# Kernel optimization log

Hardware: AMD Instinct MI355X
Metric: run time of the kernel (lower is better)

## Reference

```python
import jax, jax.numpy as jnp
import numpy as np

TEMPERATURE = 0.5
EPS = 1e-8  # matches F.cosine_similarity eps clamp


def setup_inputs() -> dict:
    key = jax.random.key(0)
    k1, k2 = jax.random.split(key)
    logits = jax.random.normal(k1, (8192, 256), dtype=jnp.float32)
    label = jax.random.randint(k2, (8192,), 0, 10, dtype=jnp.int64)
    return {"logits": logits, "label": label}


def reference(logits, label):
    n = label.shape[0]
    # pairwise cosine similarity via normalize + GEMM (same math as the
    # broadcasted F.cosine_similarity, without the O(n^2 d) intermediate)
    norms = jnp.maximum(jnp.linalg.norm(logits, axis=1, keepdims=True), EPS)
    xn = logits / norms                       # [n, d]
    sim_matrix = xn @ xn.T                    # [n, n]

    eye = jnp.eye(n, dtype=sim_matrix.dtype)
    mask = (label[:, None] == label[None, :]).astype(sim_matrix.dtype)  # same-label (incl. diag)

    e = jnp.exp(sim_matrix / TEMPERATURE) * (1.0 - eye)  # zero diagonal
    sim = mask * e                            # same-label positives
    no_sim_sum = jnp.sum(e - sim, axis=1)     # [n] row sums of different-label terms
    sim_sum = sim + no_sim_sum[:, None]       # denominator per entry
    ratio = sim / sim_sum

    # zeros (different-label entries) get +1 via (1 - mask), diagonal gets +1 via eye -> -log(1) = 0
    loss_mat = -jnp.log((1.0 - mask) + ratio + eye)
    return jnp.sum(loss_mat) / (2 * n)
```

## Files before the change

kernel.cpp:

```cpp
#include <hip/hip_runtime.h>
#include <cstdint>
#include <cstddef>

typedef __bf16 bf16x8 __attribute__((ext_vector_type(8)));
typedef float  f32x4  __attribute__((ext_vector_type(4)));

#define N_ROWS 8192
#define KDIM   256
#define TEMP_INV 2.0f
#define LOG2E  1.4426950408889634f
#define EXPC   (TEMP_INV * LOG2E)

__device__ __forceinline__ ushort f2bf(float x) {
    uint32_t u = __float_as_uint(x);
    u += 0x7fffu + ((u >> 16) & 1u);
    return (ushort)(u >> 16);
}

__global__ void build_perm(const int* __restrict__ label, int* __restrict__ perm,
                           int* __restrict__ labelPerm, int* __restrict__ classStart,
                           int* __restrict__ cumTiles)
{
    __shared__ int lcnt[256][10];
    __shared__ int cstart[11];
    __shared__ int ccount[10];
    const int tid = threadIdx.x;
    const int wave = tid >> 6, lane = tid & 63;
    const int beg = tid * 32, end = beg + 32;

    int loc[10] = {0,0,0,0,0,0,0,0,0,0};
    for (int i = beg; i < end; ++i) {
        int c = label[i]; c = (c < 0) ? 0 : (c > 9 ? 9 : c);
        loc[c]++;
    }
    #pragma unroll
    for (int c = 0; c < 10; ++c) lcnt[tid][c] = loc[c];
    __syncthreads();

    for (int c = wave; c < 10; c += 4) {
        int s0 = lcnt[lane*4+0][c], s1 = lcnt[lane*4+1][c];
        int s2 = lcnt[lane*4+2][c], s3 = lcnt[lane*4+3][c];
        int tot = s0 + s1 + s2 + s3;
        int incl = tot;
        #pragma unroll
        for (int d = 1; d < 64; d <<= 1) {
            int up = __shfl_up(incl, d, 64);
            if (lane >= d) incl += up;
        }
        int excl = incl - tot;
        lcnt[lane*4+0][c] = excl;
        lcnt[lane*4+1][c] = excl + s0;
        lcnt[lane*4+2][c] = excl + s0 + s1;
        lcnt[lane*4+3][c] = excl + s0 + s1 + s2;
        if (lane == 63) ccount[c] = incl;
    }
    __syncthreads();

    if (tid == 0) {
        int run = 0, runT = 0;
        for (int c = 0; c < 10; ++c) {
            cstart[c] = run; classStart[c] = run;
            int tpc = (ccount[c] + 127) >> 7;
            cumTiles[c] = runT;
            run  += ccount[c];
            runT += tpc * tpc;
        }
        cstart[10] = run; classStart[10] = run; cumTiles[10] = runT;
    }
    __syncthreads();

    int ofs[10];
    #pragma unroll
    for (int c = 0; c < 10; ++c) ofs[c] = lcnt[tid][c];
    for (int i = beg; i < end; ++i) {
        int c = label[i]; c = (c < 0) ? 0 : (c > 9 ? 9 : c);
        int pos = cstart[c] + ofs[c]++;
        perm[pos] = i;
        labelPerm[pos] = c;
    }
}

__global__ __launch_bounds__(256) void normalize_rows(const float* __restrict__ logits,
        const int* __restrict__ perm, ushort* __restrict__ xn)
{
    const int p = blockIdx.x * 4 + (threadIdx.x >> 6);
    const int lane = threadIdx.x & 63;
    const int old = perm[p];
    float4 v = reinterpret_cast<const float4*>(logits + (size_t)old * KDIM)[lane];
    float ss = v.x*v.x + v.y*v.y + v.z*v.z + v.w*v.w;
    #pragma unroll
    for (int off = 32; off >= 1; off >>= 1) ss += __shfl_xor(ss, off, 64);
    float inv = 1.0f / fmaxf(sqrtf(ss), 1e-8f);
    ushort4 o;
    o.x = f2bf(v.x * inv); o.y = f2bf(v.y * inv);
    o.z = f2bf(v.z * inv); o.w = f2bf(v.w * inv);
    reinterpret_cast<ushort4*>(xn + (size_t)p * KDIM)[lane] = o;
}

__device__ __forceinline__ void stage_tiles(const ushort* __restrict__ xn,
        int rowBase, int colBase, int kb, ushort* As, ushort* Bs, int wave, int lane)
{
    #pragma unroll
    for (int it = 0; it < 4; ++it) {
        int ci = it * 256 + wave * 64 + lane;
        int row = ci >> 3;
        int c = (ci & 7) ^ (row & 7);
        int rowA = rowBase + row; if (rowA > N_ROWS - 1) rowA = N_ROWS - 1;
        int rowB = colBase + row; if (rowB > N_ROWS - 1) rowB = N_ROWS - 1;
        const ushort* gA = xn + (size_t)rowA * KDIM + kb + c * 8;
        const ushort* gB = xn + (size_t)rowB * KDIM + kb + c * 8;
        ushort* lA = As + (size_t)(it * 256 + wave * 64) * 8;
        ushort* lB = Bs + (size_t)(it * 256 + wave * 64) * 8;
        __builtin_amdgcn_global_load_lds((const __attribute__((address_space(1))) void*)gA,
                                         (__attribute__((address_space(3))) void*)lA, 16, 0, 0);
        __builtin_amdgcn_global_load_lds((const __attribute__((address_space(1))) void*)gB,
                                         (__attribute__((address_space(3))) void*)lB, 16, 0, 0);
    }
}

__device__ __forceinline__ void read_frags(const ushort* As, const ushort* Bs,
        bf16x8 (&a)[2][4], bf16x8 (&b)[2][4], int wave, int lane)
{
    const int wr = wave >> 1, wc = wave & 1;
    const int lrow = lane & 15, kgrp = lane >> 4;
    #pragma unroll
    for (int kk = 0; kk < 2; ++kk) {
        const int c = kk * 4 + kgrp;
        #pragma unroll
        for (int mi = 0; mi < 4; ++mi) {
            const int row = wr*64 + mi*16 + lrow;
            a[kk][mi] = *reinterpret_cast<const bf16x8*>(As + (size_t)row * 64 + ((c ^ (row & 7)) * 8));
        }
        #pragma unroll
        for (int ni = 0; ni < 4; ++ni) {
            const int row = wc*64 + ni*16 + lrow;
            b[kk][ni] = *reinterpret_cast<const bf16x8*>(Bs + (size_t)row * 64 + ((c ^ (row & 7)) * 8));
        }
    }
}

__device__ __forceinline__ void mfma_frags(bf16x8 (&a)[2][4], bf16x8 (&b)[2][4],
                                           f32x4 (&acc)[4][4])
{
    #pragma unroll
    for (int kk = 0; kk < 2; ++kk)
        #pragma unroll
        for (int mi = 0; mi < 4; ++mi)
            #pragma unroll
            for (int ni = 0; ni < 4; ++ni)
                acc[mi][ni] = __builtin_amdgcn_mfma_f32_16x16x32_bf16(a[kk][mi], b[kk][ni], acc[mi][ni], 0, 0, 0);
}

#define PIPE_READS_RELEASE(Ac, Bc)                                   \
    bf16x8 a[2][4], b[2][4];                                         \
    read_frags(Ac, Bc, a, b, wave, lane);                            \
    __builtin_amdgcn_sched_barrier(0);                               \
    asm volatile("s_waitcnt lgkmcnt(0)" ::: "memory");               \
    __builtin_amdgcn_s_barrier();

#define PIPE_MFMA()                                                  \
    __builtin_amdgcn_s_setprio(1);                                   \
    mfma_frags(a, b, acc);                                           \
    __builtin_amdgcn_s_setprio(0);

#define PIPE_TAIL(N)                                                 \
    __builtin_amdgcn_sched_barrier(0);                               \
    asm volatile("s_waitcnt vmcnt(" #N ")" ::: "memory");            \
    __builtin_amdgcn_s_barrier();

__device__ __forceinline__ void kloop_pipe(const ushort* __restrict__ xn,
        int rowBase, int colBase, f32x4 (&acc)[4][4],
        ushort* As0, ushort* Bs0, ushort* As1, ushort* Bs1, int wave, int lane)
{
    stage_tiles(xn, rowBase, colBase, 0,  As0, Bs0, wave, lane);
    stage_tiles(xn, rowBase, colBase, 64, As1, Bs1, wave, lane);
    asm volatile("s_waitcnt vmcnt(8)" ::: "memory");
    __builtin_amdgcn_s_barrier();
    {
        PIPE_READS_RELEASE(As0, Bs0)
        stage_tiles(xn, rowBase, colBase, 128, As0, Bs0, wave, lane);
        PIPE_MFMA()
        PIPE_TAIL(8)
    }
    {
        PIPE_READS_RELEASE(As1, Bs1)
        stage_tiles(xn, rowBase, colBase, 192, As1, Bs1, wave, lane);
        PIPE_MFMA()
        PIPE_TAIL(8)
    }
    {
        PIPE_READS_RELEASE(As0, Bs0)
        PIPE_MFMA()
        PIPE_TAIL(0)
    }
    {
        PIPE_READS_RELEASE(As1, Bs1)
        PIPE_MFMA()
    }
}

__global__ __launch_bounds__(256) void phase1_gemm(const ushort* __restrict__ xn,
        const int* __restrict__ labelPerm, float* __restrict__ pD)
{
    __shared__ __align__(16) char pool[65536];
    ushort* As0 = (ushort*)(pool);
    ushort* Bs0 = (ushort*)(pool + 16384);
    ushort* As1 = (ushort*)(pool + 32768);
    ushort* Bs1 = (ushort*)(pool + 49152);
    float* rowD = (float*)(pool);
    float* colD = (float*)(pool + 16384);
    __shared__ int labLDS[256];

    const int tid = threadIdx.x;
    const int wave = tid >> 6, lane = tid & 63;

    int t = blockIdx.x, bi = 0;
    while (t >= 64 - bi) { t -= 64 - bi; ++bi; }
    const int bj = bi + t;
    const bool isDiag = (bi == bj);
    const int rowBase = bi * 128, colBase = bj * 128;

    labLDS[tid] = labelPerm[(tid < 128) ? (rowBase + tid) : (colBase + tid - 128)];
    __builtin_amdgcn_sched_barrier(0);

    f32x4 acc[4][4] = {};
    kloop_pipe(xn, rowBase, colBase, acc, As0, Bs0, As1, Bs1, wave, lane);

    const int wr = wave >> 1, wc = wave & 1;
    const int lrow = lane & 15, lgrp = lane >> 4;
    float colAcc[4] = {0.f, 0.f, 0.f, 0.f};
    #pragma unroll
    for (int mi = 0; mi < 4; ++mi) {
        #pragma unroll
        for (int reg = 0; reg < 4; ++reg) {
            const int tr = wr * 64 + mi * 16 + lgrp * 4 + reg;
            const int rl = labLDS[tr];
            float rowAcc = 0.f;
            #pragma unroll
            for (int ni = 0; ni < 4; ++ni) {
                const int tc = wc * 64 + ni * 16 + lrow;
                float e = __builtin_amdgcn_exp2f(acc[mi][ni][reg] * EXPC);
                float ed = (rl != labLDS[128 + tc]) ? e : 0.f;
                rowAcc += ed;
                colAcc[ni] += ed;
            }
            rowD[tr * 32 + wc * 16 + lrow] = rowAcc;
        }
    }
    if (!isDiag) {
        #pragma unroll
        for (int ni = 0; ni < 4; ++ni) {
            const int tc = wc * 64 + ni * 16 + lrow;
            colD[tc * 8 + wr * 4 + lgrp] = colAcc[ni];
        }
    }
    __syncthreads();

    if (tid < 128) {
        const float* p = rowD + tid * 32;
        float s = 0.f;
        #pragma unroll
        for (int k = 0; k < 8; ++k) {
            f32x4 v = *reinterpret_cast<const f32x4*>(p + k * 4);
            s += v[0] + v[1] + v[2] + v[3];
        }
        pD[(size_t)bj * N_ROWS + rowBase + tid] = s;
    } else if (!isDiag) {
        const int c2 = tid - 128;
        const float* p = colD + c2 * 8;
        f32x4 v0 = *reinterpret_cast<const f32x4*>(p);
        f32x4 v1 = *reinterpret_cast<const f32x4*>(p + 4);
        pD[(size_t)bi * N_ROWS + colBase + c2] =
            v0[0] + v0[1] + v0[2] + v0[3] + v1[0] + v1[1] + v1[2] + v1[3];
    }
}

__global__ void phase2_rowsum(const float* __restrict__ pD, float* __restrict__ Darr)
{
    const int i = blockIdx.x * blockDim.x + threadIdx.x;
    if (i >= N_ROWS) return;
    float d = 0.f;
    for (int tj = 0; tj < 64; ++tj) d += pD[(size_t)tj * N_ROWS + i];
    Darr[i] = d;
}

__global__ __launch_bounds__(256) void phase3_loss(const ushort* __restrict__ xn,
        const float* __restrict__ Darr, const int* __restrict__ classStart,
        const int* __restrict__ cumTiles, float* __restrict__ partial)
{
    __shared__ __align__(16) char pool[65536];
    ushort* As0 = (ushort*)(pool);
    ushort* Bs0 = (ushort*)(pool + 16384);
    ushort* As1 = (ushort*)(pool + 32768);
    ushort* Bs1 = (ushort*)(pool + 49152);
    __shared__ float red[256];

    const int b = blockIdx.x;
    const int nTiles = cumTiles[10];
    if (b >= nTiles) return;

    int c = 0;
    while (c < 9 && b >= cumTiles[c + 1]) ++c;
    const int s = classStart[c], e = classStart[c + 1];
    const int nc = e - s;
    const int tps = (nc + 127) >> 7;
    const int lt = b - cumTiles[c];
    const int ti = lt / tps, tj = lt - ti * tps;
    const int rowBase = s + ti * 128, colBase = s + tj * 128;

    const int tid = threadIdx.x;
    const int wave = tid >> 6, lane = tid & 63;

    f32x4 acc[4][4] = {};
    kloop_pipe(xn, rowBase, colBase, acc, As0, Bs0, As1, Bs1, wave, lane);

    const int wr = wave >> 1, wc = wave & 1;
    const int lrow = lane & 15, lgrp = lane >> 4;
    float lsum = 0.f;
    #pragma unroll
    for (int mi = 0; mi < 4; ++mi) {
        #pragma unroll
        for (int reg = 0; reg < 4; ++reg) {
            const int r = rowBase + wr * 64 + mi * 16 + lgrp * 4 + reg;
            if (r < e) {
                const float Dr = Darr[r];
                #pragma unroll
                for (int ni = 0; ni < 4; ++ni) {
                    const int cg = colBase + wc * 64 + ni * 16 + lrow;
                    if (cg < e && cg != r) {
                        float sim = acc[mi][ni][reg];
                        float ev = __builtin_amdgcn_exp2f(sim * EXPC);
                        lsum += __logf(ev + Dr) - TEMP_INV * sim;
                    }
                }
            }
        }
    }
    red[tid] = lsum;
    __syncthreads();
    for (int st = 128; st > 0; st >>= 1) {
        if (tid < st) red[tid] += red[tid + st];
        __syncthreads();
    }
    if (tid == 0) partial[b] = red[0];
}

__global__ void phase4_final(const float* __restrict__ partial, const int* __restrict__ cumTiles,
                             float* __restrict__ out)
{
    __shared__ float red[256];
    const int tid = threadIdx.x;
    const int nTiles = cumTiles[10];
    float s = 0.f;
    for (int i = tid; i < nTiles; i += 256) s += partial[i];
    red[tid] = s;
    __syncthreads();
    for (int st = 128; st > 0; st >>= 1) {
        if (tid < st) red[tid] += red[tid + st];
        __syncthreads();
    }
    if (tid == 0) out[0] = red[0] * (1.0f / 16384.0f);
}

extern "C" void kernel_launch(void* const* d_in, const int* in_sizes, int n_in,
                              void* d_out, int out_size, void* d_ws, size_t ws_size,
                              hipStream_t stream)
{
    const float* logits = (const float*)d_in[0];
    const int*   label  = (const int*)d_in[1];
    float* out = (float*)d_out;

    char* ws = (char*)d_ws;
    ushort* xn        = (ushort*)(ws);
    float*  pD        = (float*)(ws + (4u << 20));
    float*  Darr      = (float*)(ws + (6u << 20));
    int*    perm      = (int*)(ws + (6u << 20) + (64u << 10));
    int*    labelPerm = (int*)(ws + (6u << 20) + (128u << 10));
    int*    classStart= (int*)(ws + (6u << 20) + (192u << 10));
    int*    cumTiles  = (int*)(ws + (6u << 20) + (192u << 10) + 256);
    float*  partial   = (float*)(ws + (6u << 20) + (256u << 10));

    hipLaunchKernelGGL(build_perm, dim3(1), dim3(256), 0, stream,
                       label, perm, labelPerm, classStart, cumTiles);
    hipLaunchKernelGGL(normalize_rows, dim3(2048), dim3(256), 0, stream,
                       logits, perm, xn);
    hipLaunchKernelGGL(phase1_gemm, dim3(2080), dim3(256), 0, stream,
                       xn, labelPerm, pD);
    hipLaunchKernelGGL(phase2_rowsum, dim3(32), dim3(256), 0, stream,
                       pD, Darr);
    hipLaunchKernelGGL(phase3_loss, dim3(4096), dim3(256), 0, stream,
                       xn, Darr, classStart, cumTiles, partial);
    hipLaunchKernelGGL(phase4_final, dim3(1), dim3(256), 0, stream,
                       partial, cumTiles, out);
}
```

Measured before the change: 75.63 us.

## Enlarge phase1 GEMM tiles to 256x256 with 512 threads and rework build_perm

The similarity GEMM now works on 256x256 upper-triangular tiles with 8 waves per block, giving 528 blocks instead of 2080 128x128 tiles. This halves the number of partial row-sum slices read by phase2 and cuts redundant global loads. Block indices are swizzled so that blocks running together share operand rows. The diagonal is zeroed explicitly inside diagonal tiles. build_perm is widened to 1024 threads with strided label loads to shorten its serial loop. The larger tiles mean more LDS per block, more registers per wave and fewer blocks in flight.

```diff
diff --git a/kernel.cpp b/kernel.cpp
--- a/kernel.cpp
+++ b/kernel.cpp
@@ -17,41 +17,43 @@
     return (ushort)(u >> 16);
 }
 
-__global__ void build_perm(const int* __restrict__ label, int* __restrict__ perm,
-                           int* __restrict__ labelPerm, int* __restrict__ classStart,
-                           int* __restrict__ cumTiles)
-{
-    __shared__ int lcnt[256][10];
+__global__ __launch_bounds__(1024) void build_perm(const int* __restrict__ label,
+        int* __restrict__ perm, int* __restrict__ labelPerm,
+        int* __restrict__ classStart, int* __restrict__ cumTiles)
+{
+    __shared__ unsigned short lcnt[1024][10];
     __shared__ int cstart[11];
     __shared__ int ccount[10];
     const int tid = threadIdx.x;
     const int wave = tid >> 6, lane = tid & 63;
-    const int beg = tid * 32, end = beg + 32;
-
-    int loc[10] = {0,0,0,0,0,0,0,0,0,0};
-    for (int i = beg; i < end; ++i) {
-        int c = label[i]; c = (c < 0) ? 0 : (c > 9 ? 9 : c);
-        loc[c]++;
-    }
+
+    int lab[8];
+    #pragma unroll
+    for (int j = 0; j < 8; ++j) {
+        int c = label[tid + j * 1024];
+        lab[j] = (c < 0) ? 0 : (c > 9 ? 9 : c);
+    }
+    unsigned short loc[10] = {0,0,0,0,0,0,0,0,0,0};
+    #pragma unroll
+    for (int j = 0; j < 8; ++j) loc[lab[j]]++;
     #pragma unroll
     for (int c = 0; c < 10; ++c) lcnt[tid][c] = loc[c];
     __syncthreads();
 
-    for (int c = wave; c < 10; c += 4) {
-        int s0 = lcnt[lane*4+0][c], s1 = lcnt[lane*4+1][c];
-        int s2 = lcnt[lane*4+2][c], s3 = lcnt[lane*4+3][c];
-        int tot = s0 + s1 + s2 + s3;
+    if (wave < 10) {
+        const int c = wave;
+        int s[16]; int tot = 0;
+        #pragma unroll
+        for (int m = 0; m < 16; ++m) { s[m] = lcnt[lane * 16 + m][c]; tot += s[m]; }
         int incl = tot;
         #pragma unroll
         for (int d = 1; d < 64; d <<= 1) {
             int up = __shfl_up(incl, d, 64);
             if (lane >= d) incl += up;
         }
-        int excl = incl - tot;
-        lcnt[lane*4+0][c] = excl;
-        lcnt[lane*4+1][c] = excl + s0;
-        lcnt[lane*4+2][c] = excl + s0 + s1;
-        lcnt[lane*4+3][c] = excl + s0 + s1 + s2;
+        int run = incl - tot;
+        #pragma unroll
+        for (int m = 0; m < 16; ++m) { lcnt[lane * 16 + m][c] = (unsigned short)run; run += s[m]; }
         if (lane == 63) ccount[c] = incl;
     }
     __syncthreads();
@@ -72,10 +74,11 @@
     int ofs[10];
     #pragma unroll
     for (int c = 0; c < 10; ++c) ofs[c] = lcnt[tid][c];
-    for (int i = beg; i < end; ++i) {
-        int c = label[i]; c = (c < 0) ? 0 : (c > 9 ? 9 : c);
+    #pragma unroll
+    for (int j = 0; j < 8; ++j) {
+        int c = lab[j];
         int pos = cstart[c] + ofs[c]++;
-        perm[pos] = i;
+        perm[pos] = tid + j * 1024;
         labelPerm[pos] = c;
     }
 }
@@ -105,10 +108,8 @@
         int ci = it * 256 + wave * 64 + lane;
         int row = ci >> 3;
         int c = (ci & 7) ^ (row & 7);
-        int rowA = rowBase + row; if (rowA > N_ROWS - 1) rowA = N_ROWS - 1;
-        int rowB = colBase + row; if (rowB > N_ROWS - 1) rowB = N_ROWS - 1;
-        const ushort* gA = xn + (size_t)rowA * KDIM + kb + c * 8;
-        const ushort* gB = xn + (size_t)rowB * KDIM + kb + c * 8;
+        const ushort* gA = xn + (size_t)(rowBase + row) * KDIM + kb + c * 8;
+        const ushort* gB = xn + (size_t)(colBase + row) * KDIM + kb + c * 8;
         ushort* lA = As + (size_t)(it * 256 + wave * 64) * 8;
         ushort* lB = Bs + (size_t)(it * 256 + wave * 64) * 8;
         __builtin_amdgcn_global_load_lds((const __attribute__((address_space(1))) void*)gA,
@@ -156,7 +157,9 @@
     read_frags(Ac, Bc, a, b, wave, lane);                            \
     __builtin_amdgcn_sched_barrier(0);                               \
     asm volatile("s_waitcnt lgkmcnt(0)" ::: "memory");               \
-    __builtin_amdgcn_s_barrier();
+    __builtin_amdgcn_sched_barrier(0);                               \
+    __builtin_amdgcn_s_barrier();                                    \
+    __builtin_amdgcn_sched_barrier(0);
 
 #define PIPE_MFMA()                                                  \
     __builtin_amdgcn_s_setprio(1);                                   \
@@ -166,7 +169,8 @@
 #define PIPE_TAIL(N)                                                 \
     __builtin_amdgcn_sched_barrier(0);                               \
     asm volatile("s_waitcnt vmcnt(" #N ")" ::: "memory");            \
-    __builtin_amdgcn_s_barrier();
+    __builtin_amdgcn_s_barrier();                                    \
+    __builtin_amdgcn_sched_barrier(0);
 
 __device__ __forceinline__ void kloop_pipe(const ushort* __restrict__ xn,
         int rowBase, int colBase, f32x4 (&acc)[4][4],
@@ -176,6 +180,7 @@
     stage_tiles(xn, rowBase, colBase, 64, As1, Bs1, wave, lane);
     asm volatile("s_waitcnt vmcnt(8)" ::: "memory");
     __builtin_amdgcn_s_barrier();
+    __builtin_amdgcn_sched_barrier(0);
     {
         PIPE_READS_RELEASE(As0, Bs0)
         stage_tiles(xn, rowBase, colBase, 128, As0, Bs0, wave, lane);
@@ -199,78 +204,176 @@
     }
 }
 
-__global__ __launch_bounds__(256) void phase1_gemm(const ushort* __restrict__ xn,
+__device__ __forceinline__ void stage_quad(const ushort* __restrict__ xn,
+        int base, int kb, ushort* dst, int wave, int lane)
+{
+    #pragma unroll
+    for (int it = 0; it < 4; ++it) {
+        int ci = it * 512 + wave * 64 + lane;
+        int row = ci >> 3;
+        int c = (ci & 7) ^ (row & 7);
+        const ushort* g = xn + (size_t)(base + row) * KDIM + kb + c * 8;
+        ushort* l = dst + (size_t)(it * 512 + wave * 64) * 8;
+        __builtin_amdgcn_global_load_lds((const __attribute__((address_space(1))) void*)g,
+                                         (__attribute__((address_space(3))) void*)l, 16, 0, 0);
+    }
+}
+
+__device__ __forceinline__ void read_q_kk(const ushort* As, const ushort* Bs, int kk,
+        bf16x8 (&a)[8], bf16x8 (&b)[4], int wave, int lane)
+{
+    const int wr = wave >> 2, wc = wave & 3;
+    const int lrow = lane & 15, kgrp = lane >> 4;
+    const int c = kk * 4 + kgrp;
+    #pragma unroll
+    for (int mi = 0; mi < 8; ++mi) {
+        const int row = wr*128 + mi*16 + lrow;
+        a[mi] = *reinterpret_cast<const bf16x8*>(As + (size_t)row * 64 + ((c ^ (row & 7)) * 8));
+    }
+    #pragma unroll
+    for (int ni = 0; ni < 4; ++ni) {
+        const int row = wc*64 + ni*16 + lrow;
+        b[ni] = *reinterpret_cast<const bf16x8*>(Bs + (size_t)row * 64 + ((c ^ (row & 7)) * 8));
+    }
+}
+
+__device__ __forceinline__ void mfma_q_kk(bf16x8 (&a)[8], bf16x8 (&b)[4], f32x4 (&acc)[8][4])
+{
+    #pragma unroll
+    for (int mi = 0; mi < 8; ++mi)
+        #pragma unroll
+        for (int ni = 0; ni < 4; ++ni)
+            acc[mi][ni] = __builtin_amdgcn_mfma_f32_16x16x32_bf16(a[mi], b[ni], acc[mi][ni], 0, 0, 0);
+}
+
+#define QSTEP(Acur, Bcur, DO_STAGE, STAGE_KB, VM)                    \
+    {                                                                 \
+        bf16x8 a0[8], b0[4], a1[8], b1[4];                            \
+        read_q_kk(Acur, Bcur, 0, a0, b0, wave, lane);                 \
+        __builtin_amdgcn_s_setprio(1);                                \
+        mfma_q_kk(a0, b0, acc);                                       \
+        __builtin_amdgcn_s_setprio(0);                                \
+        read_q_kk(Acur, Bcur, 1, a1, b1, wave, lane);                 \
+        __builtin_amdgcn_sched_barrier(0);                            \
+        asm volatile("s_waitcnt lgkmcnt(0)" ::: "memory");            \
+        __builtin_amdgcn_sched_barrier(0);                            \
+        __builtin_amdgcn_s_barrier();                                 \
+        __builtin_amdgcn_sched_barrier(0);                            \
+        if (DO_STAGE) {                                               \
+            stage_quad(xn, rowBase, STAGE_KB, Acur, wave, lane);      \
+            stage_quad(xn, colBase, STAGE_KB, Bcur, wave, lane);      \
+        }                                                             \
+        __builtin_amdgcn_s_setprio(1);                                \
+        mfma_q_kk(a1, b1, acc);                                       \
+        __builtin_amdgcn_s_setprio(0);                                \
+        __builtin_amdgcn_sched_barrier(0);                            \
+        asm volatile("s_waitcnt vmcnt(" VM ")" ::: "memory");         \
+        __builtin_amdgcn_s_barrier();                                 \
+        __builtin_amdgcn_sched_barrier(0);                            \
+    }
+
+__global__ __launch_bounds__(512, 2) void phase1_gemm(const ushort* __restrict__ xn,
         const int* __restrict__ labelPerm, float* __restrict__ pD)
 {
-    __shared__ __align__(16) char pool[65536];
+    __shared__ __align__(16) char pool[131072];
+    __shared__ float colD[256][8];
+    __shared__ int labq[512];
     ushort* As0 = (ushort*)(pool);
-    ushort* Bs0 = (ushort*)(pool + 16384);
-    ushort* As1 = (ushort*)(pool + 32768);
-    ushort* Bs1 = (ushort*)(pool + 49152);
-    float* rowD = (float*)(pool);
-    float* colD = (float*)(pool + 16384);
-    __shared__ int labLDS[256];
+    ushort* Bs0 = (ushort*)(pool + 32768);
+    ushort* As1 = (ushort*)(pool + 65536);
+    ushort* Bs1 = (ushort*)(pool + 98304);
+    float* rowD = (float*)pool;
 
     const int tid = threadIdx.x;
     const int wave = tid >> 6, lane = tid & 63;
 
-    int t = blockIdx.x, bi = 0;
-    while (t >= 64 - bi) { t -= 64 - bi; ++bi; }
-    const int bj = bi + t;
-    const bool isDiag = (bi == bj);
-    const int rowBase = bi * 128, colBase = bj * 128;
-
-    labLDS[tid] = labelPerm[(tid < 128) ? (rowBase + tid) : (colBase + tid - 128)];
+    int bIdx = (int)blockIdx.x;
+    int sw = (bIdx & 7) * 66 + (bIdx >> 3);
+    int t2 = sw, Bi = 0;
+    while (t2 >= 32 - Bi) { t2 -= 32 - Bi; ++Bi; }
+    const int Bj = Bi + t2;
+    const bool isDiag = (Bi == Bj);
+    const int rowBase = Bi * 256, colBase = Bj * 256;
+
+    labq[tid] = labelPerm[(tid < 256) ? (rowBase + tid) : (colBase + tid - 256)];
     __builtin_amdgcn_sched_barrier(0);
 
-    f32x4 acc[4][4] = {};
-    kloop_pipe(xn, rowBase, colBase, acc, As0, Bs0, As1, Bs1, wave, lane);
-
-    const int wr = wave >> 1, wc = wave & 1;
+    f32x4 acc[8][4] = {};
+
+    stage_quad(xn, rowBase, 0,  As0, wave, lane);
+    stage_quad(xn, colBase, 0,  Bs0, wave, lane);
+    stage_quad(xn, rowBase, 64, As1, wave, lane);
+    stage_quad(xn, colBase, 64, Bs1, wave, lane);
+    asm volatile("s_waitcnt vmcnt(8)" ::: "memory");
+    __builtin_amdgcn_s_barrier();
+    __builtin_amdgcn_sched_barrier(0);
+
+    QSTEP(As0, Bs0, true, 128, "8")
+    QSTEP(As1, Bs1, true, 192, "8")
+    QSTEP(As0, Bs0, false, 0, "0")
+    {
+        bf16x8 a0[8], b0[4], a1[8], b1[4];
+        read_q_kk(As1, Bs1, 0, a0, b0, wave, lane);
+        __builtin_amdgcn_s_setprio(1);
+        mfma_q_kk(a0, b0, acc);
+        __builtin_amdgcn_s_setprio(0);
+        read_q_kk(As1, Bs1, 1, a1, b1, wave, lane);
+        __builtin_amdgcn_sched_barrier(0);
+        asm volatile("s_waitcnt lgkmcnt(0)" ::: "memory");
+        __builtin_amdgcn_sched_barrier(0);
+        __builtin_amdgcn_s_barrier();
+        __builtin_amdgcn_sched_barrier(0);
+        __builtin_amdgcn_s_setprio(1);
+        mfma_q_kk(a1, b1, acc);
+        __builtin_amdgcn_s_setprio(0);
+    }
+
+    const int wr = wave >> 2, wc = wave & 3;
     const int lrow = lane & 15, lgrp = lane >> 4;
     float colAcc[4] = {0.f, 0.f, 0.f, 0.f};
     #pragma unroll
-    for (int mi = 0; mi < 4; ++mi) {
+    for (int mi = 0; mi < 8; ++mi) {
         #pragma unroll
         for (int reg = 0; reg < 4; ++reg) {
-            const int tr = wr * 64 + mi * 16 + lgrp * 4 + reg;
-            const int rl = labLDS[tr];
+            const int tr = wr * 128 + mi * 16 + lgrp * 4 + reg;
+            const int rl = labq[tr];
             float rowAcc = 0.f;
             #pragma unroll
             for (int ni = 0; ni < 4; ++ni) {
                 const int tc = wc * 64 + ni * 16 + lrow;
                 float e = __builtin_amdgcn_exp2f(acc[mi][ni][reg] * EXPC);
-                float ed = (rl != labLDS[128 + tc]) ? e : 0.f;
+                if (isDiag && tr == tc) e = 0.f;
+                float ed = (rl != labq[256 + tc]) ? e : 0.f;
                 rowAcc += ed;
                 colAcc[ni] += ed;
             }
-            rowD[tr * 32 + wc * 16 + lrow] = rowAcc;
+            rowD[tr * 68 + wc * 16 + lrow] = rowAcc;
         }
     }
     if (!isDiag) {
         #pragma unroll
         for (int ni = 0; ni < 4; ++ni) {
             const int tc = wc * 64 + ni * 16 + lrow;
-            colD[tc * 8 + wr * 4 + lgrp] = colAcc[ni];
-        }
-    }
-    __syncthreads();
-
-    if (tid < 128) {
-        const float* p = rowD + tid * 32;
+            colD[tc][wr * 4 + lgrp] = colAcc[ni];
+        }
+    }
+    __syncthreads();
+
+    if (tid < 256) {
+        const float* p = rowD + tid * 68;
         float s = 0.f;
         #pragma unroll
-        for (int k = 0; k < 8; ++k) {
+        for (int k = 0; k < 16; ++k) {
             f32x4 v = *reinterpret_cast<const f32x4*>(p + k * 4);
             s += v[0] + v[1] + v[2] + v[3];
         }
-        pD[(size_t)bj * N_ROWS + rowBase + tid] = s;
+        pD[(size_t)Bj * N_ROWS + rowBase + tid] = s;
     } else if (!isDiag) {
-        const int c2 = tid - 128;
-        const float* p = colD + c2 * 8;
+        const int c2 = tid - 256;
+        const float* p = &colD[c2][0];
         f32x4 v0 = *reinterpret_cast<const f32x4*>(p);
         f32x4 v1 = *reinterpret_cast<const f32x4*>(p + 4);
-        pD[(size_t)bi * N_ROWS + colBase + c2] =
+        pD[(size_t)Bi * N_ROWS + colBase + c2] =
             v0[0] + v0[1] + v0[2] + v0[3] + v1[0] + v1[1] + v1[2] + v1[3];
     }
 }
@@ -280,7 +383,7 @@
     const int i = blockIdx.x * blockDim.x + threadIdx.x;
     if (i >= N_ROWS) return;
     float d = 0.f;
-    for (int tj = 0; tj < 64; ++tj) d += pD[(size_t)tj * N_ROWS + i];
+    for (int tj = 0; tj < 32; ++tj) d += pD[(size_t)tj * N_ROWS + i];
     Darr[i] = d;
 }
 
@@ -380,11 +483,11 @@
     int*    cumTiles  = (int*)(ws + (6u << 20) + (192u << 10) + 256);
     float*  partial   = (float*)(ws + (6u << 20) + (256u << 10));
 
-    hipLaunchKernelGGL(build_perm, dim3(1), dim3(256), 0, stream,
+    hipLaunchKernelGGL(build_perm, dim3(1), dim3(1024), 0, stream,
                        label, perm, labelPerm, classStart, cumTiles);
     hipLaunchKernelGGL(normalize_rows, dim3(2048), dim3(256), 0, stream,
                        logits, perm, xn);
-    hipLaunchKernelGGL(phase1_gemm, dim3(2080), dim3(256), 0, stream,
+    hipLaunchKernelGGL(phase1_gemm, dim3(528), dim3(512), 0, stream,
                        xn, labelPerm, pD);
     hipLaunchKernelGGL(phase2_rowsum, dim3(32), dim3(256), 0, stream,
                        pD, Darr);
```

Result: slower. 77.15 us (+2.0%).

## Fuse all phases into one persistent cooperative kernel with grid syncs

Applied to the files above, without the earlier changes.

Replaces the six separate launches (perm build, normalize, tile GEMM row-sum, row-sum reduce, loss GEMM, final reduce) with one cooperative persistent kernel. Phases are separated by grid.sync(), and the final reduction is done by the last block to finish, detected with an atomic counter. The per-row denominator reduction is folded into the loss phase, so each tile sums pD into LDS. This removes launch gaps and the Darr round trip. In exchange, the grid is limited to the number of co-resident blocks, phases run with grid-stride loops, grid barriers are added, and the single-block perm build now stalls the whole grid.

```diff
diff --git a/kernel.cpp b/kernel.cpp
--- a/kernel.cpp
+++ b/kernel.cpp
@@ -1,6 +1,9 @@
 #include <hip/hip_runtime.h>
+#include <hip/hip_cooperative_groups.h>
 #include <cstdint>
 #include <cstddef>
+
+namespace cg = cooperative_groups;
 
 typedef __bf16 bf16x8 __attribute__((ext_vector_type(8)));
 typedef float  f32x4  __attribute__((ext_vector_type(4)));
@@ -17,86 +20,6 @@
     return (ushort)(u >> 16);
 }
 
-__global__ void build_perm(const int* __restrict__ label, int* __restrict__ perm,
-                           int* __restrict__ labelPerm, int* __restrict__ classStart,
-                           int* __restrict__ cumTiles)
-{
-    __shared__ int lcnt[256][10];
-    __shared__ int cstart[11];
-    __shared__ int ccount[10];
-    const int tid = threadIdx.x;
-    const int wave = tid >> 6, lane = tid & 63;
-    const int beg = tid * 32, end = beg + 32;
-
-    int loc[10] = {0,0,0,0,0,0,0,0,0,0};
-    for (int i = beg; i < end; ++i) {
-        int c = label[i]; c = (c < 0) ? 0 : (c > 9 ? 9 : c);
-        loc[c]++;
-    }
-    #pragma unroll
-    for (int c = 0; c < 10; ++c) lcnt[tid][c] = loc[c];
-    __syncthreads();
-
-    for (int c = wave; c < 10; c += 4) {
-        int s0 = lcnt[lane*4+0][c], s1 = lcnt[lane*4+1][c];
-        int s2 = lcnt[lane*4+2][c], s3 = lcnt[lane*4+3][c];
-        int tot = s0 + s1 + s2 + s3;
-        int incl = tot;
-        #pragma unroll
-        for (int d = 1; d < 64; d <<= 1) {
-            int up = __shfl_up(incl, d, 64);
-            if (lane >= d) incl += up;
-        }
-        int excl = incl - tot;
-        lcnt[lane*4+0][c] = excl;
-        lcnt[lane*4+1][c] = excl + s0;
-        lcnt[lane*4+2][c] = excl + s0 + s1;
-        lcnt[lane*4+3][c] = excl + s0 + s1 + s2;
-        if (lane == 63) ccount[c] = incl;
-    }
-    __syncthreads();
-
-    if (tid == 0) {
-        int run = 0, runT = 0;
-        for (int c = 0; c < 10; ++c) {
-            cstart[c] = run; classStart[c] = run;
-            int tpc = (ccount[c] + 127) >> 7;
-            cumTiles[c] = runT;
-            run  += ccount[c];
-            runT += tpc * tpc;
-        }
-        cstart[10] = run; classStart[10] = run; cumTiles[10] = runT;
-    }
-    __syncthreads();
-
-    int ofs[10];
-    #pragma unroll
-    for (int c = 0; c < 10; ++c) ofs[c] = lcnt[tid][c];
-    for (int i = beg; i < end; ++i) {
-        int c = label[i]; c = (c < 0) ? 0 : (c > 9 ? 9 : c);
-        int pos = cstart[c] + ofs[c]++;
-        perm[pos] = i;
-        labelPerm[pos] = c;
-    }
-}
-
-__global__ __launch_bounds__(256) void normalize_rows(const float* __restrict__ logits,
-        const int* __restrict__ perm, ushort* __restrict__ xn)
-{
-    const int p = blockIdx.x * 4 + (threadIdx.x >> 6);
-    const int lane = threadIdx.x & 63;
-    const int old = perm[p];
-    float4 v = reinterpret_cast<const float4*>(logits + (size_t)old * KDIM)[lane];
-    float ss = v.x*v.x + v.y*v.y + v.z*v.z + v.w*v.w;
-    #pragma unroll
-    for (int off = 32; off >= 1; off >>= 1) ss += __shfl_xor(ss, off, 64);
-    float inv = 1.0f / fmaxf(sqrtf(ss), 1e-8f);
-    ushort4 o;
-    o.x = f2bf(v.x * inv); o.y = f2bf(v.y * inv);
-    o.z = f2bf(v.z * inv); o.w = f2bf(v.w * inv);
-    reinterpret_cast<ushort4*>(xn + (size_t)p * KDIM)[lane] = o;
-}
-
 __device__ __forceinline__ void stage_tiles(const ushort* __restrict__ xn,
         int rowBase, int colBase, int kb, ushort* As, ushort* Bs, int wave, int lane)
 {
@@ -105,10 +28,8 @@
         int ci = it * 256 + wave * 64 + lane;
         int row = ci >> 3;
         int c = (ci & 7) ^ (row & 7);
-        int rowA = rowBase + row; if (rowA > N_ROWS - 1) rowA = N_ROWS - 1;
-        int rowB = colBase + row; if (rowB > N_ROWS - 1) rowB = N_ROWS - 1;
-        const ushort* gA = xn + (size_t)rowA * KDIM + kb + c * 8;
-        const ushort* gB = xn + (size_t)rowB * KDIM + kb + c * 8;
+        const ushort* gA = xn + (size_t)(rowBase + row) * KDIM + kb + c * 8;
+        const ushort* gB = xn + (size_t)(colBase + row) * KDIM + kb + c * 8;
         ushort* lA = As + (size_t)(it * 256 + wave * 64) * 8;
         ushort* lB = Bs + (size_t)(it * 256 + wave * 64) * 8;
         __builtin_amdgcn_global_load_lds((const __attribute__((address_space(1))) void*)gA,
@@ -156,7 +77,9 @@
     read_frags(Ac, Bc, a, b, wave, lane);                            \
     __builtin_amdgcn_sched_barrier(0);                               \
     asm volatile("s_waitcnt lgkmcnt(0)" ::: "memory");               \
-    __builtin_amdgcn_s_barrier();
+    __builtin_amdgcn_sched_barrier(0);                               \
+    __builtin_amdgcn_s_barrier();                                    \
+    __builtin_amdgcn_sched_barrier(0);
 
 #define PIPE_MFMA()                                                  \
     __builtin_amdgcn_s_setprio(1);                                   \
@@ -166,7 +89,8 @@
 #define PIPE_TAIL(N)                                                 \
     __builtin_amdgcn_sched_barrier(0);                               \
     asm volatile("s_waitcnt vmcnt(" #N ")" ::: "memory");            \
-    __builtin_amdgcn_s_barrier();
+    __builtin_amdgcn_s_barrier();                                    \
+    __builtin_amdgcn_sched_barrier(0);
 
 __device__ __forceinline__ void kloop_pipe(const ushort* __restrict__ xn,
         int rowBase, int colBase, f32x4 (&acc)[4][4],
@@ -176,6 +100,7 @@
     stage_tiles(xn, rowBase, colBase, 64, As1, Bs1, wave, lane);
     asm volatile("s_waitcnt vmcnt(8)" ::: "memory");
     __builtin_amdgcn_s_barrier();
+    __builtin_amdgcn_sched_barrier(0);
     {
         PIPE_READS_RELEASE(As0, Bs0)
         stage_tiles(xn, rowBase, colBase, 128, As0, Bs0, wave, lane);
@@ -199,167 +124,245 @@
     }
 }
 
-__global__ __launch_bounds__(256) void phase1_gemm(const ushort* __restrict__ xn,
-        const int* __restrict__ labelPerm, float* __restrict__ pD)
-{
+__global__ __launch_bounds__(256) void fused_all(const float* __restrict__ logits,
+        const int* __restrict__ label, float* __restrict__ out,
+        ushort* __restrict__ xn, float* __restrict__ pD,
+        int* __restrict__ perm, int* __restrict__ labelPerm,
+        int* __restrict__ classStartG, int* __restrict__ cumTilesG,
+        float* __restrict__ partial, unsigned int* __restrict__ counter)
+{
+    cg::grid_group grid = cg::this_grid();
+
     __shared__ __align__(16) char pool[65536];
+    __shared__ int   labLDS[256];
+    __shared__ float redF[256];
+    __shared__ float DarrL[128];
+    __shared__ int   cstart[11];
+    __shared__ int   ccount[10];
+    __shared__ int   lastFlag;
+
     ushort* As0 = (ushort*)(pool);
     ushort* Bs0 = (ushort*)(pool + 16384);
     ushort* As1 = (ushort*)(pool + 32768);
     ushort* Bs1 = (ushort*)(pool + 49152);
-    float* rowD = (float*)(pool);
+    float* rowD = (float*)pool;
     float* colD = (float*)(pool + 16384);
-    __shared__ int labLDS[256];
 
     const int tid = threadIdx.x;
     const int wave = tid >> 6, lane = tid & 63;
-
-    int t = blockIdx.x, bi = 0;
-    while (t >= 64 - bi) { t -= 64 - bi; ++bi; }
-    const int bj = bi + t;
-    const bool isDiag = (bi == bj);
-    const int rowBase = bi * 128, colBase = bj * 128;
-
-    labLDS[tid] = labelPerm[(tid < 128) ? (rowBase + tid) : (colBase + tid - 128)];
-    __builtin_amdgcn_sched_barrier(0);
-
-    f32x4 acc[4][4] = {};
-    kloop_pipe(xn, rowBase, colBase, acc, As0, Bs0, As1, Bs1, wave, lane);
-
-    const int wr = wave >> 1, wc = wave & 1;
-    const int lrow = lane & 15, lgrp = lane >> 4;
-    float colAcc[4] = {0.f, 0.f, 0.f, 0.f};
-    #pragma unroll
-    for (int mi = 0; mi < 4; ++mi) {
-        #pragma unroll
-        for (int reg = 0; reg < 4; ++reg) {
-            const int tr = wr * 64 + mi * 16 + lgrp * 4 + reg;
-            const int rl = labLDS[tr];
-            float rowAcc = 0.f;
+    const int bid = blockIdx.x, nb = gridDim.x;
+
+    if (bid == 0) {
+        int* lcnt = (int*)pool;
+        const int beg = tid * 32, end = beg + 32;
+        int loc[10] = {0,0,0,0,0,0,0,0,0,0};
+        for (int i = beg; i < end; ++i) {
+            int c = label[i]; c = (c < 0) ? 0 : (c > 9 ? 9 : c);
+            loc[c]++;
+        }
+        #pragma unroll
+        for (int c = 0; c < 10; ++c) lcnt[tid * 10 + c] = loc[c];
+        if (tid == 0) counter[0] = 0u;
+        __syncthreads();
+
+        for (int c = wave; c < 10; c += 4) {
+            int s0 = lcnt[(lane*4+0)*10 + c], s1 = lcnt[(lane*4+1)*10 + c];
+            int s2 = lcnt[(lane*4+2)*10 + c], s3 = lcnt[(lane*4+3)*10 + c];
+            int tot = s0 + s1 + s2 + s3;
+            int incl = tot;
+            #pragma unroll
+            for (int d = 1; d < 64; d <<= 1) {
+                int up = __shfl_up(incl, d, 64);
+                if (lane >= d) incl += up;
+            }
+            int excl = incl - tot;
+            lcnt[(lane*4+0)*10 + c] = excl;
+            lcnt[(lane*4+1)*10 + c] = excl + s0;
+            lcnt[(lane*4+2)*10 + c] = excl + s0 + s1;
+            lcnt[(lane*4+3)*10 + c] = excl + s0 + s1 + s2;
+            if (lane == 63) ccount[c] = incl;
+        }
+        __syncthreads();
+
+        if (tid == 0) {
+            int run = 0, runT = 0;
+            for (int c = 0; c < 10; ++c) {
+                cstart[c] = run; classStartG[c] = run;
+                int tpc = (ccount[c] + 127) >> 7;
+                cumTilesG[c] = runT;
+                run  += ccount[c];
+                runT += tpc * tpc;
+            }
+            classStartG[10] = run; cumTilesG[10] = runT;
+        }
+        __syncthreads();
+
+        int ofs[10];
+        #pragma unroll
+        for (int c = 0; c < 10; ++c) ofs[c] = lcnt[tid * 10 + c];
+        for (int i = beg; i < end; ++i) {
+            int c = label[i]; c = (c < 0) ? 0 : (c > 9 ? 9 : c);
+            int pos = cstart[c] + ofs[c]++;
+            perm[pos] = i;
+            labelPerm[pos] = c;
+        }
+    }
+    grid.sync();
+
+    for (int g = bid; g < N_ROWS / 4; g += nb) {
+        const int pos = g * 4 + wave;
+        const int old = perm[pos];
+        float4 v = reinterpret_cast<const float4*>(logits + (size_t)old * KDIM)[lane];
+        float ss = v.x*v.x + v.y*v.y + v.z*v.z + v.w*v.w;
+        #pragma unroll
+        for (int off = 32; off >= 1; off >>= 1) ss += __shfl_xor(ss, off, 64);
+        float inv = 1.0f / fmaxf(sqrtf(ss), 1e-8f);
+        ushort4 o;
+        o.x = f2bf(v.x * inv); o.y = f2bf(v.y * inv);
+        o.z = f2bf(v.z * inv); o.w = f2bf(v.w * inv);
+        reinterpret_cast<ushort4*>(xn + (size_t)pos * KDIM)[lane] = o;
+    }
+    grid.sync();
+
+    for (int t = bid; t < 2080; t += nb) {
+        int tt = t, bi = 0;
+        while (tt >= 64 - bi) { tt -= 64 - bi; ++bi; }
+        const int bj = bi + tt;
+        const bool isDiag = (bi == bj);
+        const int rowBase = bi * 128, colBase = bj * 128;
+
+        labLDS[tid] = labelPerm[(tid < 128) ? (rowBase + tid) : (colBase + tid - 128)];
+        __builtin_amdgcn_sched_barrier(0);
+
+        f32x4 acc[4][4] = {};
+        kloop_pipe(xn, rowBase, colBase, acc, As0, Bs0, As1, Bs1, wave, lane);
+
+        const int wr = wave >> 1, wc = wave & 1;
+        const int lrow = lane & 15, lgrp = lane >> 4;
+        float colAcc[4] = {0.f, 0.f, 0.f, 0.f};
+        #pragma unroll
+        for (int mi = 0; mi < 4; ++mi) {
+            #pragma unroll
+            for (int reg = 0; reg < 4; ++reg) {
+                const int tr = wr * 64 + mi * 16 + lgrp * 4 + reg;
+                const int rl = labLDS[tr];
+                float rowAcc = 0.f;
+                #pragma unroll
+                for (int ni = 0; ni < 4; ++ni) {
+                    const int tc = wc * 64 + ni * 16 + lrow;
+                    float e = __builtin_amdgcn_exp2f(acc[mi][ni][reg] * EXPC);
+                    float ed = (rl != labLDS[128 + tc]) ? e : 0.f;
+                    rowAcc += ed;
+                    colAcc[ni] += ed;
+                }
+                rowD[tr * 32 + wc * 16 + lrow] = rowAcc;
+            }
+        }
+        if (!isDiag) {
             #pragma unroll
             for (int ni = 0; ni < 4; ++ni) {
                 const int tc = wc * 64 + ni * 16 + lrow;
-                float e = __builtin_amdgcn_exp2f(acc[mi][ni][reg] * EXPC);
-                float ed = (rl != labLDS[128 + tc]) ? e : 0.f;
-                rowAcc += ed;
-                colAcc[ni] += ed;
-            }
-            rowD[tr * 32 + wc * 16 + lrow] = rowAcc;
-        }
-    }
-    if (!isDiag) {
-        #pragma unroll
-        for (int ni = 0; ni < 4; ++ni) {
-            const int tc = wc * 64 + ni * 16 + lrow;
-            colD[tc * 8 + wr * 4 + lgrp] = colAcc[ni];
-        }
-    }
+                colD[tc * 8 + wr * 4 + lgrp] = colAcc[ni];
+            }
+        }
+        __syncthreads();
+
+        if (tid < 128) {
+            const float* p = rowD + tid * 32;
+            float s = 0.f;
+            #pragma unroll
+            for (int k = 0; k < 8; ++k) {
+                f32x4 v = *reinterpret_cast<const f32x4*>(p + k * 4);
+                s += v[0] + v[1] + v[2] + v[3];
+            }
+            pD[(size_t)bj * N_ROWS + rowBase + tid] = s;
+        } else if (!isDiag) {
+            const int c2 = tid - 128;
+            const float* p = colD + c2 * 8;
+            f32x4 v0 = *reinterpret_cast<const f32x4*>(p);
+            f32x4 v1 = *reinterpret_cast<const f32x4*>(p + 4);
+            pD[(size_t)bi * N_ROWS + colBase + c2] =
+                v0[0] + v0[1] + v0[2] + v0[3] + v1[0] + v1[1] + v1[2] + v1[3];
+        }
+        __syncthreads();
+    }
+    grid.sync();
+
+    if (tid < 11) { labLDS[tid] = classStartG[tid]; labLDS[32 + tid] = cumTilesG[tid]; }
     __syncthreads();
-
-    if (tid < 128) {
-        const float* p = rowD + tid * 32;
-        float s = 0.f;
-        #pragma unroll
-        for (int k = 0; k < 8; ++k) {
-            f32x4 v = *reinterpret_cast<const f32x4*>(p + k * 4);
-            s += v[0] + v[1] + v[2] + v[3];
-        }
-        pD[(size_t)bj * N_ROWS + rowBase + tid] = s;
-    } else if (!isDiag) {
-        const int c2 = tid - 128;
-        const float* p = colD + c2 * 8;
-        f32x4 v0 = *reinterpret_cast<const f32x4*>(p);
-        f32x4 v1 = *reinterpret_cast<const f32x4*>(p + 4);
-        pD[(size_t)bi * N_ROWS + colBase + c2] =
-            v0[0] + v0[1] + v0[2] + v0[3] + v1[0] + v1[1] + v1[2] + v1[3];
-    }
-}
-
-__global__ void phase2_rowsum(const float* __restrict__ pD, float* __restrict__ Darr)
-{
-    const int i = blockIdx.x * blockDim.x + threadIdx.x;
-    if (i >= N_ROWS) return;
-    float d = 0.f;
-    for (int tj = 0; tj < 64; ++tj) d += pD[(size_t)tj * N_ROWS + i];
-    Darr[i] = d;
-}
-
-__global__ __launch_bounds__(256) void phase3_loss(const ushort* __restrict__ xn,
-        const float* __restrict__ Darr, const int* __restrict__ classStart,
-        const int* __restrict__ cumTiles, float* __restrict__ partial)
-{
-    __shared__ __align__(16) char pool[65536];
-    ushort* As0 = (ushort*)(pool);
-    ushort* Bs0 = (ushort*)(pool + 16384);
-    ushort* As1 = (ushort*)(pool + 32768);
-    ushort* Bs1 = (ushort*)(pool + 49152);
-    __shared__ float red[256];
-
-    const int b = blockIdx.x;
-    const int nTiles = cumTiles[10];
-    if (b >= nTiles) return;
-
-    int c = 0;
-    while (c < 9 && b >= cumTiles[c + 1]) ++c;
-    const int s = classStart[c], e = classStart[c + 1];
-    const int nc = e - s;
-    const int tps = (nc + 127) >> 7;
-    const int lt = b - cumTiles[c];
-    const int ti = lt / tps, tj = lt - ti * tps;
-    const int rowBase = s + ti * 128, colBase = s + tj * 128;
-
-    const int tid = threadIdx.x;
-    const int wave = tid >> 6, lane = tid & 63;
-
-    f32x4 acc[4][4] = {};
-    kloop_pipe(xn, rowBase, colBase, acc, As0, Bs0, As1, Bs1, wave, lane);
-
-    const int wr = wave >> 1, wc = wave & 1;
-    const int lrow = lane & 15, lgrp = lane >> 4;
-    float lsum = 0.f;
-    #pragma unroll
-    for (int mi = 0; mi < 4; ++mi) {
-        #pragma unroll
-        for (int reg = 0; reg < 4; ++reg) {
-            const int r = rowBase + wr * 64 + mi * 16 + lgrp * 4 + reg;
-            if (r < e) {
-                const float Dr = Darr[r];
-                #pragma unroll
-                for (int ni = 0; ni < 4; ++ni) {
-                    const int cg = colBase + wc * 64 + ni * 16 + lrow;
-                    if (cg < e && cg != r) {
-                        float sim = acc[mi][ni][reg];
-                        float ev = __builtin_amdgcn_exp2f(sim * EXPC);
-                        lsum += __logf(ev + Dr) - TEMP_INV * sim;
+    const int nTiles = labLDS[32 + 10];
+
+    for (int t = bid; t < nTiles; t += nb) {
+        int c = 0;
+        while (c < 9 && t >= labLDS[32 + c + 1]) ++c;
+        const int s = labLDS[c], e = labLDS[c + 1];
+        const int nc = e - s;
+        const int tps = (nc + 127) >> 7;
+        const int lt = t - labLDS[32 + c];
+        const int ti = lt / tps, tj = lt - ti * tps;
+        const int rowBase = s + ti * 128, colBase = s + tj * 128;
+
+        if (tid < 128) {
+            float d = 0.f;
+            for (int sl = 0; sl < 64; ++sl) d += pD[(size_t)sl * N_ROWS + rowBase + tid];
+            DarrL[tid] = d;
+        }
+        __syncthreads();
+
+        f32x4 acc[4][4] = {};
+        kloop_pipe(xn, rowBase, colBase, acc, As0, Bs0, As1, Bs1, wave, lane);
+
+        const int wr = wave >> 1, wc = wave & 1;
+        const int lrow = lane & 15, lgrp = lane >> 4;
+        float lsum = 0.f;
+        #pragma unroll
+        for (int mi = 0; mi < 4; ++mi) {
+            #pragma unroll
+            for (int reg = 0; reg < 4; ++reg) {
+                const int tr = wr * 64 + mi * 16 + lgrp * 4 + reg;
+                const int r = rowBase + tr;
+                if (r < e) {
+                    const float Dr = DarrL[tr];
+                    #pragma unroll
+                    for (int ni = 0; ni < 4; ++ni) {
+                        const int cg2 = colBase + wc * 64 + ni * 16 + lrow;
+                        if (cg2 < e && cg2 != r) {
+                            float sim = acc[mi][ni][reg];
+                            float ev = __builtin_amdgcn_exp2f(sim * EXPC);
+                            lsum += __logf(ev + Dr) - TEMP_INV * sim;
+                        }
                     }
                 }
             }
         }
-    }
-    red[tid] = lsum;
+        redF[tid] = lsum;
+        __syncthreads();
+        for (int st = 128; st > 0; st >>= 1) {
+            if (tid < st) redF[tid] += redF[tid + st];
+            __syncthreads();
+        }
+        if (tid == 0) partial[t] = redF[0];
+        __syncthreads();
+    }
+
+    __threadfence();
+    if (tid == 0) {
+        unsigned int old = atomicAdd(counter, 1u);
+        lastFlag = (old == (unsigned int)(nb - 1)) ? 1 : 0;
+    }
     __syncthreads();
-    for (int st = 128; st > 0; st >>= 1) {
-        if (tid < st) red[tid] += red[tid + st];
-        __syncthreads();
-    }
-    if (tid == 0) partial[b] = red[0];
-}
-
-__global__ void phase4_final(const float* __restrict__ partial, const int* __restrict__ cumTiles,
-                             float* __restrict__ out)
-{
-    __shared__ float red[256];
-    const int tid = threadIdx.x;
-    const int nTiles = cumTiles[10];
-    float s = 0.f;
-    for (int i = tid; i < nTiles; i += 256) s += partial[i];
-    red[tid] = s;
-    __syncthreads();
-    for (int st = 128; st > 0; st >>= 1) {
-        if (tid < st) red[tid] += red[tid + st];
-        __syncthreads();
-    }
-    if (tid == 0) out[0] = red[0] * (1.0f / 16384.0f);
+    if (lastFlag) {
+        __threadfence();
+        float s = 0.f;
+        for (int i = tid; i < nTiles; i += 256) s += partial[i];
+        redF[tid] = s;
+        __syncthreads();
+        for (int st = 128; st > 0; st >>= 1) {
+            if (tid < st) redF[tid] += redF[tid + st];
+            __syncthreads();
+        }
+        if (tid == 0) out[0] = redF[0] * (1.0f / 16384.0f);
+    }
 }
 
 extern "C" void kernel_launch(void* const* d_in, const int* in_sizes, int n_in,
@@ -371,25 +374,28 @@
     float* out = (float*)d_out;
 
     char* ws = (char*)d_ws;
-    ushort* xn        = (ushort*)(ws);
-    float*  pD        = (float*)(ws + (4u << 20));
-    float*  Darr      = (float*)(ws + (6u << 20));
-    int*    perm      = (int*)(ws + (6u << 20) + (64u << 10));
-    int*    labelPerm = (int*)(ws + (6u << 20) + (128u << 10));
-    int*    classStart= (int*)(ws + (6u << 20) + (192u << 10));
-    int*    cumTiles  = (int*)(ws + (6u << 20) + (192u << 10) + 256);
-    float*  partial   = (float*)(ws + (6u << 20) + (256u << 10));
-
-    hipLaunchKernelGGL(build_perm, dim3(1), dim3(256), 0, stream,
-                       label, perm, labelPerm, classStart, cumTiles);
-    hipLaunchKernelGGL(normalize_rows, dim3(2048), dim3(256), 0, stream,
-                       logits, perm, xn);
-    hipLaunchKernelGGL(phase1_gemm, dim3(2080), dim3(256), 0, stream,
-                       xn, labelPerm, pD);
-    hipLaunchKernelGGL(phase2_rowsum, dim3(32), dim3(256), 0, stream,
-                       pD, Darr);
-    hipLaunchKernelGGL(phase3_loss, dim3(4096), dim3(256), 0, stream,
-                       xn, Darr, classStart, cumTiles, partial);
-    hipLaunchKernelGGL(phase4_final, dim3(1), dim3(256), 0, stream,
-                       partial, cumTiles, out);
-}
+    ushort*       xn         = (ushort*)(ws);
+    float*        pD         = (float*)(ws + (4u << 20));
+    int*          perm       = (int*)(ws + (6u << 20));
+    int*          labelPerm  = (int*)(ws + (6u << 20) + (32u << 10));
+    int*          classStartG= (int*)(ws + (6u << 20) + (64u << 10));
+    int*          cumTilesG  = (int*)(ws + (6u << 20) + (64u << 10) + 256);
+    float*        partial    = (float*)(ws + (6u << 20) + (128u << 10));
+    unsigned int* counter    = (unsigned int*)(ws + (6u << 20) + (192u << 10));
+
+    int occ = 0;
+    hipOccupancyMaxActiveBlocksPerMultiprocessor(&occ, fused_all, 256, 0);
+    if (occ < 1) occ = 1;
+    int ncu = 0;
+    hipDeviceGetAttribute(&ncu, hipDeviceAttributeMultiprocessorCount, 0);
+    if (ncu < 1) ncu = 256;
+    int nb = occ * ncu;
+    if (nb > 512) nb = 512;
+
+    void* kargs[] = {
+        (void*)&logits, (void*)&label, (void*)&out,
+        (void*)&xn, (void*)&pD, (void*)&perm, (void*)&labelPerm,
+        (void*)&classStartG, (void*)&cumTilesG, (void*)&partial, (void*)&counter
+    };
+    hipLaunchCooperativeKernel(fused_all, dim3(nb), dim3(256), kargs, 0, stream);
+}
```

Result: slower. 194.2 us (+156.7%).
